# Performance work log

Hardware: AMD Instinct MI355X
Metric: run time of the kernel (lower is better)

The kernel has to match this reference:

```python
import jax, jax.numpy as jnp
import numpy as np

LOG2PI = float(np.log(2.0 * np.pi))


def setup_inputs() -> dict:
    key = jax.random.key(0)
    ks = jax.random.split(key, 5)
    B, T, XD, C = 128, 2050, 6, 64
    return {
        "x": jax.random.normal(ks[0], (B, T, XD), jnp.float32),
        "observation_means": jax.random.uniform(ks[1], (C, XD), dtype=jnp.float32),
        "observation_stddevs": jax.random.uniform(ks[2], (C, XD), dtype=jnp.float32),
        "log_A": jax.random.normal(ks[3], (C, C), jnp.float32),
        "log_pi": jax.random.normal(ks[4], (C,), jnp.float32),
    }


def _emission_logprob(x, means, stds):
    # Normal(means[:, :4], relu(stds[:, :4]) + 0.1).log_prob(x[:, :, :4]) summed over feat dim
    mu = means[:, :4]                       # (C,4)
    sigma = jax.nn.relu(stds[:, :4]) + 0.1  # (C,4)
    z = (x[:, :, None, :4] - mu) / sigma    # (B,T,C,4)
    return jnp.sum(-0.5 * z * z - jnp.log(sigma) - 0.5 * LOG2PI, axis=-1)  # (B,T,C)


def _forward_scalers(logp, log_A, log_pi):
    # scaled HMM forward pass; returns per-step log normalizers (T,B)
    a0 = logp[:, 0] + log_pi
    s0 = jax.nn.logsumexp(a0, axis=-1)
    a0n = a0 - s0[:, None]

    def step(a_prev, lp_t):
        a = lp_t + jax.nn.logsumexp(a_prev[:, :, None] + log_A[None], axis=1)
        s = jax.nn.logsumexp(a, axis=-1)
        return a - s[:, None], s

    _, s_rest = jax.lax.scan(step, a0n, jnp.swapaxes(logp[:, 1:], 0, 1))
    return jnp.concatenate([s0[None], s_rest], axis=0)  # (T,B)


def _viterbi(logp, log_A, log_pi):
    d0 = logp[:, 0] + log_pi  # (B,C)

    def step(d_prev, lp_t):
        scores = d_prev[:, :, None] + log_A[None]  # (B,C_prev,C_cur)
        psi_t = jnp.argmax(scores, axis=1)
        d = jnp.max(scores, axis=1) + lp_t
        return d, psi_t

    d_last, psi = jax.lax.scan(step, d0, jnp.swapaxes(logp[:, 1:], 0, 1))  # psi: (T-1,B,C)
    c_last = jnp.argmax(d_last, axis=-1)  # (B,)

    def back(c_next, psi_t):
        c_t = jnp.take_along_axis(psi_t, c_next[:, None], axis=1)[:, 0]
        return c_t, c_t

    _, cs = jax.lax.scan(back, c_last, psi, reverse=True)  # (T-1,B)
    c = jnp.concatenate([cs, c_last[None]], axis=0)  # (T,B)
    return jnp.swapaxes(c, 0, 1)  # (B,T)


def reference(x, observation_means, observation_stddevs, log_A, log_pi):
    logA = jax.nn.log_softmax(log_A, axis=1)
    logpi = jax.nn.log_softmax(log_pi, axis=0)
    logp = _emission_logprob(x, observation_means, observation_stddevs)  # (B,T,C)
    scalers = _forward_scalers(logp, logA, logpi)                         # (T,B)
    logp_x = jnp.sum(scalers, axis=0)                                     # (B,)
    c_est = _viterbi(logp, logA, logpi)                                   # (B,T) int
    return logp_x, c_est
```

## Files before the change

kernel.cpp:

```cpp
#include <hip/hip_runtime.h>

#define T_LEN 2050
#define B_SZ 128
#define NCHUNK 33
#define HL2PI 0.91893853320467274178f

__device__ __forceinline__ float waveMax(float v) {
#pragma unroll
    for (int off = 32; off >= 1; off >>= 1)
        v = fmaxf(v, __shfl_xor(v, off, 64));
    return v;
}
__device__ __forceinline__ float waveSum(float v) {
#pragma unroll
    for (int off = 32; off >= 1; off >>= 1)
        v += __shfl_xor(v, off, 64);
    return v;
}
__device__ __forceinline__ void waveArgmax(float& v, int& idx) {
#pragma unroll
    for (int off = 32; off >= 1; off >>= 1) {
        float ov = __shfl_xor(v, off, 64);
        int   oi = __shfl_xor(idx, off, 64);
        if (ov > v || (ov == v && oi < idx)) { v = ov; idx = oi; }
    }
}
__device__ __forceinline__ void cfence() { asm volatile("" ::: "memory"); }

__device__ __forceinline__ float dppSumAll(float v) {
#define SSTEP(ctrl) { int t_ = __builtin_amdgcn_update_dpp(0, __float_as_int(v), ctrl, 0xf, 0xf, true); \
                      v = v + __int_as_float(t_); }
    SSTEP(0x111) SSTEP(0x112) SSTEP(0x114) SSTEP(0x118) SSTEP(0x142) SSTEP(0x143)
#undef SSTEP
    return __int_as_float(__builtin_amdgcn_readlane(__float_as_int(v), 63));
}
__device__ __forceinline__ float dppMaxAll(float v) {
#define MSTEP(ctrl) { int t_ = __builtin_amdgcn_update_dpp(__float_as_int(v), __float_as_int(v), ctrl, 0xf, 0xf, false); \
                      v = fmaxf(v, __int_as_float(t_)); }
    MSTEP(0x111) MSTEP(0x112) MSTEP(0x114) MSTEP(0x118) MSTEP(0x142) MSTEP(0x143)
#undef MSTEP
    return __int_as_float(__builtin_amdgcn_readlane(__float_as_int(v), 63));
}

extern "C" __global__ __launch_bounds__(64, 1)
void hmm_prep(const float* __restrict__ logA_in,
              const float* __restrict__ logpi_in,
              float* __restrict__ lAg,
              float* __restrict__ lpig)
{
    __shared__ float la[64 * 65];
    __shared__ float rowlse[64];
    const int j = threadIdx.x;
#pragma unroll
    for (int k = 0; k < 64; ++k)
        la[k * 65 + j] = logA_in[k * 64 + j];
    cfence();
    {
        float m = -1e30f;
#pragma unroll
        for (int k = 0; k < 64; ++k) m = fmaxf(m, la[j * 65 + k]);
        float s = 0.f;
#pragma unroll
        for (int k = 0; k < 64; ++k) s += expf(la[j * 65 + k] - m);
        rowlse[j] = m + logf(s);
    }
    cfence();
    {
        float v = logpi_in[j];
        float m = waveMax(v);
        float s = waveSum(expf(v - m));
        lpig[j] = v - (m + logf(s));
    }
    float4* o = (float4*)lAg;
#pragma unroll
    for (int k = 0; k < 16; ++k) {
        float4 v;
        v.x = la[(4 * k + 0) * 65 + j] - rowlse[4 * k + 0];
        v.y = la[(4 * k + 1) * 65 + j] - rowlse[4 * k + 1];
        v.z = la[(4 * k + 2) * 65 + j] - rowlse[4 * k + 2];
        v.w = la[(4 * k + 3) * 65 + j] - rowlse[4 * k + 3];
        o[j * 16 + k] = v;
    }
}

extern "C" __global__ __launch_bounds__(64, 1)
void hmm_main(const float* __restrict__ x,
              const float* __restrict__ means,
              const float* __restrict__ stds,
              const float* __restrict__ lAg,
              const float* __restrict__ lpig,
              float* __restrict__ out,
              float* __restrict__ dstore,
              int* __restrict__ c_last)
{
    __shared__ __align__(16) float xs[12304];
    __shared__ __align__(16) float pbuf[64];

    const int j   = threadIdx.x;
    const int bid = blockIdx.x;
    const bool is_fwd = (bid < B_SZ);
    const int b = is_fwd ? bid : bid - B_SZ;

    {
        const float4* xg4 = (const float4*)(x + (size_t)b * T_LEN * 6);
        float4* xs4 = (float4*)xs;
        for (int i = j; i < 3075; i += 64) xs4[i] = xg4[i];
    }
    float lpi = lpig[j];

    float mu0 = means[j * 6 + 0], mu1 = means[j * 6 + 1];
    float mu2 = means[j * 6 + 2], mu3 = means[j * 6 + 3];
    float sg0 = fmaxf(stds[j * 6 + 0], 0.f) + 0.1f;
    float sg1 = fmaxf(stds[j * 6 + 1], 0.f) + 0.1f;
    float sg2 = fmaxf(stds[j * 6 + 2], 0.f) + 0.1f;
    float sg3 = fmaxf(stds[j * 6 + 3], 0.f) + 0.1f;
    float ls0 = logf(sg0), ls1 = logf(sg1), ls2 = logf(sg2), ls3 = logf(sg3);

    const float4* pv = (const float4*)pbuf;

    if (is_fwd) {
        float Ac[64];
        {
            const float4* g = (const float4*)lAg;
#pragma unroll
            for (int k = 0; k < 16; ++k) {
                float4 v = g[j * 16 + k];
                Ac[4 * k + 0] = __expf(v.x); Ac[4 * k + 1] = __expf(v.y);
                Ac[4 * k + 2] = __expf(v.z); Ac[4 * k + 3] = __expf(v.w);
            }
        }
        float i0 = 1.f / sg0, i1 = 1.f / sg1, i2 = 1.f / sg2, i3 = 1.f / sg3;
        float cst = -(ls0 + ls1 + ls2 + ls3) - 4.f * HL2PI;

        float z0 = (xs[0] - mu0) * i0, z1 = (xs[1] - mu1) * i1;
        float z2 = (xs[2] - mu2) * i2, z3 = (xs[3] - mu3) * i3;
        float a0 = (cst - 0.5f * (z0 * z0 + z1 * z1 + z2 * z2 + z3 * z3)) + lpi;
        float mm0 = dppMaxAll(a0);
        float u0 = __expf(a0 - mm0);
        pbuf[j] = u0;
        float4 rr[16];
#pragma unroll
        for (int k = 0; k < 16; ++k) rr[k] = pv[k];
        float s0 = dppSumAll(u0);
        double acc = (double)(mm0 + __logf(s0));
        float rcp = 1.0f / s0;
        float lp1;
        {
            float y0 = (xs[6] - mu0) * i0, y1 = (xs[7] - mu1) * i1;
            float y2 = (xs[8] - mu2) * i2, y3 = (xs[9] - mu3) * i3;
            lp1 = cst - 0.5f * (y0 * y0 + y1 * y1 + y2 * y2 + y3 * y3);
        }
        float mm_c = dppMaxAll(lp1);
        float e_c  = __expf(lp1 - mm_c) * rcp;

#pragma unroll 1
        for (int t = 1; t < T_LEN; ++t) {
            int o = ((t + 1 < T_LEN) ? (t + 1) : t) * 6;
            float y0 = xs[o], y1 = xs[o + 1], y2 = xs[o + 2], y3 = xs[o + 3];

            float q0 = 0.f, q1 = 0.f, q2 = 0.f, q3 = 0.f;
#pragma unroll
            for (int k = 0; k < 16; ++k) {
                float4 pp = rr[k];
                q0 = fmaf(pp.x, Ac[4 * k + 0], q0);
                q1 = fmaf(pp.y, Ac[4 * k + 1], q1);
                q2 = fmaf(pp.z, Ac[4 * k + 2], q2);
                q3 = fmaf(pp.w, Ac[4 * k + 3], q3);
            }
            float q = (q0 + q1) + (q2 + q3);
            float u = q * e_c;

            pbuf[j] = u;
#pragma unroll
            for (int k = 0; k < 16; ++k) rr[k] = pv[k];

            float s = dppSumAll(u);
            acc += (double)(mm_c + __logf(s));
            rcp = 1.0f / s;
            float w0 = (y0 - mu0) * i0, w1 = (y1 - mu1) * i1;
            float w2 = (y2 - mu2) * i2, w3 = (y3 - mu3) * i3;
            float lpn = cst - 0.5f * (w0 * w0 + w1 * w1 + w2 * w2 + w3 * w3);
            float mmn = dppMaxAll(lpn);
            e_c  = __expf(lpn - mmn) * rcp;
            mm_c = mmn;
        }
        if (j == 0) out[b] = (float)acc;
    } else {
        float lA[64];
        {
            const float4* g = (const float4*)lAg;
#pragma unroll
            for (int k = 0; k < 16; ++k) {
                float4 v = g[j * 16 + k];
                lA[4 * k + 0] = v.x; lA[4 * k + 1] = v.y;
                lA[4 * k + 2] = v.z; lA[4 * k + 3] = v.w;
            }
        }
        float z0 = (xs[0] - mu0) / sg0, z1 = (xs[1] - mu1) / sg1;
        float z2 = (xs[2] - mu2) / sg2, z3 = (xs[3] - mu3) / sg3;
        float e0 = ((-0.5f * z0) * z0 - ls0) - HL2PI;
        float e1 = ((-0.5f * z1) * z1 - ls1) - HL2PI;
        float e2 = ((-0.5f * z2) * z2 - ls2) - HL2PI;
        float e3 = ((-0.5f * z3) * z3 - ls3) - HL2PI;
        float dn = (((e0 + e1) + e2) + e3) + lpi;
        pbuf[j] = dn;
        float4 rr[16];
#pragma unroll
        for (int k = 0; k < 16; ++k) rr[k] = pv[k];
        float* dp = dstore + (size_t)b * 64 + j;
        *dp = dn;
        float lp_c;
        {
            float y0 = (xs[6] - mu0) / sg0, y1 = (xs[7] - mu1) / sg1;
            float y2 = (xs[8] - mu2) / sg2, y3 = (xs[9] - mu3) / sg3;
            float f0 = ((-0.5f * y0) * y0 - ls0) - HL2PI;
            float f1 = ((-0.5f * y1) * y1 - ls1) - HL2PI;
            float f2 = ((-0.5f * y2) * y2 - ls2) - HL2PI;
            float f3 = ((-0.5f * y3) * y3 - ls3) - HL2PI;
            lp_c = ((f0 + f1) + f2) + f3;
        }

#pragma unroll 1
        for (int t = 1; t < T_LEN; ++t) {
            int o = ((t + 1 < T_LEN) ? (t + 1) : t) * 6;
            float y0 = xs[o], y1 = xs[o + 1], y2 = xs[o + 2], y3 = xs[o + 3];

            float m0 = -3.4e38f, m1 = -3.4e38f, m2 = -3.4e38f, m3 = -3.4e38f;
#pragma unroll
            for (int k = 0; k < 16; ++k) {
                float4 dd = rr[k];
                m0 = fmaxf(m0, dd.x + lA[4 * k + 0]);
                m1 = fmaxf(m1, dd.y + lA[4 * k + 1]);
                m2 = fmaxf(m2, dd.z + lA[4 * k + 2]);
                m3 = fmaxf(m3, dd.w + lA[4 * k + 3]);
            }
            float best = fmaxf(fmaxf(m0, m1), fmaxf(m2, m3));
            dn = best + lp_c;

            pbuf[j] = dn;
#pragma unroll
            for (int k = 0; k < 16; ++k) rr[k] = pv[k];

            dp += B_SZ * 64;
            *dp = dn;
            float w0 = (y0 - mu0) / sg0, w1 = (y1 - mu1) / sg1;
            float w2 = (y2 - mu2) / sg2, w3 = (y3 - mu3) / sg3;
            float f0 = ((-0.5f * w0) * w0 - ls0) - HL2PI;
            float f1 = ((-0.5f * w1) * w1 - ls1) - HL2PI;
            float f2 = ((-0.5f * w2) * w2 - ls2) - HL2PI;
            float f3 = ((-0.5f * w3) * w3 - ls3) - HL2PI;
            lp_c = ((f0 + f1) + f2) + f3;
        }

        float vv = dn; int idx = j;
        waveArgmax(vv, idx);
        if (j == 0) c_last[b] = idx;
    }
}

extern "C" __global__ __launch_bounds__(256)
void hmm_psi(const float* __restrict__ dstore,
             const float* __restrict__ lAg,
             unsigned char* __restrict__ psi)
{
    __shared__ __align__(16) float sd[4][64];
    const int warp = threadIdx.x >> 6;
    const int j = threadIdx.x & 63;
    const int wid = blockIdx.x * 4 + warp;

    float lA[64];
    {
        const float4* g = (const float4*)lAg;
#pragma unroll
        for (int k = 0; k < 16; ++k) {
            float4 v = g[j * 16 + k];
            lA[4 * k + 0] = v.x; lA[4 * k + 1] = v.y;
            lA[4 * k + 2] = v.z; lA[4 * k + 3] = v.w;
        }
    }
    const float4* dv = (const float4*)sd[warp];
    const int NP = 2049 * B_SZ;

    for (int p = wid; p < NP; p += 2048) {
        const int t = (p >> 7) + 1;
        const int b = p & 127;
        float dval = dstore[((size_t)(t - 1) * B_SZ + b) * 64 + j];
        sd[warp][j] = dval;

        float bv0 = -3.4e38f, bv1 = -3.4e38f, bv2 = -3.4e38f, bv3 = -3.4e38f;
        int bi0 = 0, bi1 = 1, bi2 = 2, bi3 = 3;
#pragma unroll
        for (int k = 0; k < 16; ++k) {
            float4 dd = dv[k];
            float v0 = dd.x + lA[4 * k + 0];
            float v1 = dd.y + lA[4 * k + 1];
            float v2 = dd.z + lA[4 * k + 2];
            float v3 = dd.w + lA[4 * k + 3];
            if (v0 > bv0) { bv0 = v0; bi0 = 4 * k + 0; }
            if (v1 > bv1) { bv1 = v1; bi1 = 4 * k + 1; }
            if (v2 > bv2) { bv2 = v2; bi2 = 4 * k + 2; }
            if (v3 > bv3) { bv3 = v3; bi3 = 4 * k + 3; }
        }
        float best = bv0; int bidx = bi0;
        if (bv1 > best || (bv1 == best && bi1 < bidx)) { best = bv1; bidx = bi1; }
        if (bv2 > best || (bv2 == best && bi2 < bidx)) { best = bv2; bidx = bi2; }
        if (bv3 > best || (bv3 == best && bi3 < bidx)) { best = bv3; bidx = bi3; }

        psi[((size_t)t * B_SZ + b) * 64 + j] = (unsigned char)bidx;
    }
}

extern "C" __global__ __launch_bounds__(256)
void hmm_compose(const unsigned char* __restrict__ psi,
                 unsigned char* __restrict__ mt)
{
    const int w = blockIdx.x * 4 + (threadIdx.x >> 6);
    const int j = threadIdx.x & 63;
    const int g = w % NCHUNK;
    const int b = w / NCHUNK;
    const int e = (g < NCHUNK - 1) ? g * 64 + 64 : (T_LEN - 1);
    int M = j;
    for (int t = e; t >= g * 64 + 1; --t)
        M = psi[((size_t)t * B_SZ + b) * 64 + M];
    mt[((size_t)g * B_SZ + b) * 64 + j] = (unsigned char)M;
}

extern "C" __global__ __launch_bounds__(64, 1)
void hmm_fill(const unsigned char* __restrict__ psi,
              const unsigned char* __restrict__ mt,
              const int* __restrict__ c_last,
              float* __restrict__ out)
{
    __shared__ int sb[NCHUNK];
    const int b = blockIdx.x;
    const int g = threadIdx.x;
    const int cl = c_last[b];
    if (g == 0) {
        int cur = cl;
        for (int q = NCHUNK - 1; q >= 0; --q) {
            cur = mt[((size_t)q * B_SZ + b) * 64 + cur];
            sb[q] = cur;
        }
    }
    cfence();
    float* oc = out + B_SZ + (size_t)b * T_LEN;
    if (g == NCHUNK) {
        oc[T_LEN - 1] = (float)cl;
    } else if (g < NCHUNK) {
        const int e = (g < NCHUNK - 1) ? g * 64 + 64 : (T_LEN - 1);
        int s = (g < NCHUNK - 1) ? sb[g + 1] : cl;
        for (int t = e; t >= g * 64 + 1; --t) {
            s = psi[((size_t)t * B_SZ + b) * 64 + s];
            oc[t - 1] = (float)s;
        }
    }
}

extern "C" void kernel_launch(void* const* d_in, const int* in_sizes, int n_in,
                              void* d_out, int out_size, void* d_ws, size_t ws_size,
                              hipStream_t stream)
{
    const float* x      = (const float*)d_in[0];
    const float* means  = (const float*)d_in[1];
    const float* stds   = (const float*)d_in[2];
    const float* logA   = (const float*)d_in[3];
    const float* logpi  = (const float*)d_in[4];
    float* out = (float*)d_out;

    char* base = (char*)d_ws;
    float*         dstore = (float*)base;
    unsigned char* psi    = (unsigned char*)(base + 67174400);
    unsigned char* mt     = (unsigned char*)(base + 83968000);
    int*           cl     = (int*)(base + 84238336);
    float*         lAg    = (float*)(base + 84238848);
    float*         lpig   = (float*)(base + 84255232);

    hipLaunchKernelGGL(hmm_prep, dim3(1), dim3(64), 0, stream, logA, logpi, lAg, lpig);
    hipLaunchKernelGGL(hmm_main, dim3(2 * B_SZ), dim3(64), 0, stream,
                       x, means, stds, lAg, lpig, out, dstore, cl);
    hipLaunchKernelGGL(hmm_psi, dim3(512), dim3(256), 0, stream, dstore, lAg, psi);
    hipLaunchKernelGGL(hmm_compose, dim3((NCHUNK * B_SZ) / 4), dim3(256), 0, stream, psi, mt);
    hipLaunchKernelGGL(hmm_fill, dim3(B_SZ), dim3(64), 0, stream, psi, mt, cl, out);
}
```

Measured before the change: 1.078 ms.

## Fuse forward and Viterbi recurrences into one wave per batch; widen psi grid

```diff
diff --git a/kernel.cpp b/kernel.cpp
--- a/kernel.cpp
+++ b/kernel.cpp
@@ -94,12 +94,11 @@
               int* __restrict__ c_last)
 {
     __shared__ __align__(16) float xs[12304];
-    __shared__ __align__(16) float pbuf[64];
-
-    const int j   = threadIdx.x;
-    const int bid = blockIdx.x;
-    const bool is_fwd = (bid < B_SZ);
-    const int b = is_fwd ? bid : bid - B_SZ;
+    __shared__ __align__(16) float fbuf[64];
+    __shared__ __align__(16) float vbuf[64];
+
+    const int j = threadIdx.x;
+    const int b = blockIdx.x;
 
     {
         const float4* xg4 = (const float4*)(x + (size_t)b * T_LEN * 6);
@@ -116,146 +115,126 @@
     float sg3 = fmaxf(stds[j * 6 + 3], 0.f) + 0.1f;
     float ls0 = logf(sg0), ls1 = logf(sg1), ls2 = logf(sg2), ls3 = logf(sg3);
 
-    const float4* pv = (const float4*)pbuf;
-
-    if (is_fwd) {
-        float Ac[64];
-        {
-            const float4* g = (const float4*)lAg;
-#pragma unroll
-            for (int k = 0; k < 16; ++k) {
-                float4 v = g[j * 16 + k];
-                Ac[4 * k + 0] = __expf(v.x); Ac[4 * k + 1] = __expf(v.y);
-                Ac[4 * k + 2] = __expf(v.z); Ac[4 * k + 3] = __expf(v.w);
-            }
-        }
-        float i0 = 1.f / sg0, i1 = 1.f / sg1, i2 = 1.f / sg2, i3 = 1.f / sg3;
-        float cst = -(ls0 + ls1 + ls2 + ls3) - 4.f * HL2PI;
-
-        float z0 = (xs[0] - mu0) * i0, z1 = (xs[1] - mu1) * i1;
-        float z2 = (xs[2] - mu2) * i2, z3 = (xs[3] - mu3) * i3;
-        float a0 = (cst - 0.5f * (z0 * z0 + z1 * z1 + z2 * z2 + z3 * z3)) + lpi;
-        float mm0 = dppMaxAll(a0);
-        float u0 = __expf(a0 - mm0);
-        pbuf[j] = u0;
-        float4 rr[16];
-#pragma unroll
-        for (int k = 0; k < 16; ++k) rr[k] = pv[k];
-        float s0 = dppSumAll(u0);
-        double acc = (double)(mm0 + __logf(s0));
-        float rcp = 1.0f / s0;
-        float lp1;
-        {
-            float y0 = (xs[6] - mu0) * i0, y1 = (xs[7] - mu1) * i1;
-            float y2 = (xs[8] - mu2) * i2, y3 = (xs[9] - mu3) * i3;
-            lp1 = cst - 0.5f * (y0 * y0 + y1 * y1 + y2 * y2 + y3 * y3);
-        }
-        float mm_c = dppMaxAll(lp1);
-        float e_c  = __expf(lp1 - mm_c) * rcp;
+    float lA[64], Ac[64];
+    {
+        const float4* g = (const float4*)lAg;
+#pragma unroll
+        for (int k = 0; k < 16; ++k) {
+            float4 v = g[j * 16 + k];
+            lA[4 * k + 0] = v.x; lA[4 * k + 1] = v.y;
+            lA[4 * k + 2] = v.z; lA[4 * k + 3] = v.w;
+        }
+#pragma unroll
+        for (int k = 0; k < 64; ++k) Ac[k] = __expf(lA[k]);
+    }
+    float i0 = 1.f / sg0, i1 = 1.f / sg1, i2 = 1.f / sg2, i3 = 1.f / sg3;
+    float cst = -(ls0 + ls1 + ls2 + ls3) - 4.f * HL2PI;
+
+    const float4* fv = (const float4*)fbuf;
+    const float4* vv = (const float4*)vbuf;
+
+    float z0 = (xs[0] - mu0) * i0, z1 = (xs[1] - mu1) * i1;
+    float z2 = (xs[2] - mu2) * i2, z3 = (xs[3] - mu3) * i3;
+    float a0 = (cst - 0.5f * (z0 * z0 + z1 * z1 + z2 * z2 + z3 * z3)) + lpi;
+    float mm0 = dppMaxAll(a0);
+    float u = __expf(a0 - mm0);
+    fbuf[j] = u;
+    float v0 = (xs[0] - mu0) / sg0, v1 = (xs[1] - mu1) / sg1;
+    float v2 = (xs[2] - mu2) / sg2, v3 = (xs[3] - mu3) / sg3;
+    float e0 = ((-0.5f * v0) * v0 - ls0) - HL2PI;
+    float e1 = ((-0.5f * v1) * v1 - ls1) - HL2PI;
+    float e2 = ((-0.5f * v2) * v2 - ls2) - HL2PI;
+    float e3 = ((-0.5f * v3) * v3 - ls3) - HL2PI;
+    float dn = (((e0 + e1) + e2) + e3) + lpi;
+    vbuf[j] = dn;
+
+    float4 fr[16], vr[16];
+#pragma unroll
+    for (int k = 0; k < 16; ++k) fr[k] = fv[k];
+#pragma unroll
+    for (int k = 0; k < 16; ++k) vr[k] = vv[k];
+
+    float s0 = dppSumAll(u);
+    double acc = (double)(mm0 + __logf(s0));
+    float rcp = 1.0f / s0;
+    float* dp = dstore + (size_t)b * 64 + j;
+    *dp = dn;
+
+    float lp_f, mm_c, e_c, lp_v;
+    {
+        float y0 = xs[6], y1 = xs[7], y2 = xs[8], y3 = xs[9];
+        float w0 = (y0 - mu0) * i0, w1 = (y1 - mu1) * i1;
+        float w2 = (y2 - mu2) * i2, w3 = (y3 - mu3) * i3;
+        lp_f = cst - 0.5f * (w0 * w0 + w1 * w1 + w2 * w2 + w3 * w3);
+        mm_c = dppMaxAll(lp_f);
+        e_c  = __expf(lp_f - mm_c) * rcp;
+        float q0 = (y0 - mu0) / sg0, q1 = (y1 - mu1) / sg1;
+        float q2 = (y2 - mu2) / sg2, q3 = (y3 - mu3) / sg3;
+        float f0 = ((-0.5f * q0) * q0 - ls0) - HL2PI;
+        float f1 = ((-0.5f * q1) * q1 - ls1) - HL2PI;
+        float f2 = ((-0.5f * q2) * q2 - ls2) - HL2PI;
+        float f3 = ((-0.5f * q3) * q3 - ls3) - HL2PI;
+        lp_v = ((f0 + f1) + f2) + f3;
+    }
 
 #pragma unroll 1
-        for (int t = 1; t < T_LEN; ++t) {
-            int o = ((t + 1 < T_LEN) ? (t + 1) : t) * 6;
-            float y0 = xs[o], y1 = xs[o + 1], y2 = xs[o + 2], y3 = xs[o + 3];
-
-            float q0 = 0.f, q1 = 0.f, q2 = 0.f, q3 = 0.f;
-#pragma unroll
-            for (int k = 0; k < 16; ++k) {
-                float4 pp = rr[k];
-                q0 = fmaf(pp.x, Ac[4 * k + 0], q0);
-                q1 = fmaf(pp.y, Ac[4 * k + 1], q1);
-                q2 = fmaf(pp.z, Ac[4 * k + 2], q2);
-                q3 = fmaf(pp.w, Ac[4 * k + 3], q3);
-            }
-            float q = (q0 + q1) + (q2 + q3);
-            float u = q * e_c;
-
-            pbuf[j] = u;
-#pragma unroll
-            for (int k = 0; k < 16; ++k) rr[k] = pv[k];
-
-            float s = dppSumAll(u);
-            acc += (double)(mm_c + __logf(s));
-            rcp = 1.0f / s;
-            float w0 = (y0 - mu0) * i0, w1 = (y1 - mu1) * i1;
-            float w2 = (y2 - mu2) * i2, w3 = (y3 - mu3) * i3;
-            float lpn = cst - 0.5f * (w0 * w0 + w1 * w1 + w2 * w2 + w3 * w3);
-            float mmn = dppMaxAll(lpn);
-            e_c  = __expf(lpn - mmn) * rcp;
-            mm_c = mmn;
-        }
-        if (j == 0) out[b] = (float)acc;
-    } else {
-        float lA[64];
-        {
-            const float4* g = (const float4*)lAg;
-#pragma unroll
-            for (int k = 0; k < 16; ++k) {
-                float4 v = g[j * 16 + k];
-                lA[4 * k + 0] = v.x; lA[4 * k + 1] = v.y;
-                lA[4 * k + 2] = v.z; lA[4 * k + 3] = v.w;
-            }
-        }
-        float z0 = (xs[0] - mu0) / sg0, z1 = (xs[1] - mu1) / sg1;
-        float z2 = (xs[2] - mu2) / sg2, z3 = (xs[3] - mu3) / sg3;
-        float e0 = ((-0.5f * z0) * z0 - ls0) - HL2PI;
-        float e1 = ((-0.5f * z1) * z1 - ls1) - HL2PI;
-        float e2 = ((-0.5f * z2) * z2 - ls2) - HL2PI;
-        float e3 = ((-0.5f * z3) * z3 - ls3) - HL2PI;
-        float dn = (((e0 + e1) + e2) + e3) + lpi;
-        pbuf[j] = dn;
-        float4 rr[16];
-#pragma unroll
-        for (int k = 0; k < 16; ++k) rr[k] = pv[k];
-        float* dp = dstore + (size_t)b * 64 + j;
+    for (int t = 1; t < T_LEN; ++t) {
+        int o = ((t + 1 < T_LEN) ? (t + 1) : t) * 6;
+        float y0 = xs[o], y1 = xs[o + 1], y2 = xs[o + 2], y3 = xs[o + 3];
+
+        float m0 = -3.4e38f, m1 = -3.4e38f, m2 = -3.4e38f, m3 = -3.4e38f;
+#pragma unroll
+        for (int k = 0; k < 16; ++k) {
+            float4 dd = vr[k];
+            m0 = fmaxf(m0, dd.x + lA[4 * k + 0]);
+            m1 = fmaxf(m1, dd.y + lA[4 * k + 1]);
+            m2 = fmaxf(m2, dd.z + lA[4 * k + 2]);
+            m3 = fmaxf(m3, dd.w + lA[4 * k + 3]);
+        }
+        dn = fmaxf(fmaxf(m0, m1), fmaxf(m2, m3)) + lp_v;
+
+        float q0 = 0.f, q1 = 0.f, q2 = 0.f, q3 = 0.f;
+#pragma unroll
+        for (int k = 0; k < 16; ++k) {
+            float4 pp = fr[k];
+            q0 = fmaf(pp.x, Ac[4 * k + 0], q0);
+            q1 = fmaf(pp.y, Ac[4 * k + 1], q1);
+            q2 = fmaf(pp.z, Ac[4 * k + 2], q2);
+            q3 = fmaf(pp.w, Ac[4 * k + 3], q3);
+        }
+        u = ((q0 + q1) + (q2 + q3)) * e_c;
+
+        vbuf[j] = dn;
+        fbuf[j] = u;
+#pragma unroll
+        for (int k = 0; k < 16; ++k) vr[k] = vv[k];
+#pragma unroll
+        for (int k = 0; k < 16; ++k) fr[k] = fv[k];
+
+        dp += B_SZ * 64;
         *dp = dn;
-        float lp_c;
-        {
-            float y0 = (xs[6] - mu0) / sg0, y1 = (xs[7] - mu1) / sg1;
-            float y2 = (xs[8] - mu2) / sg2, y3 = (xs[9] - mu3) / sg3;
-            float f0 = ((-0.5f * y0) * y0 - ls0) - HL2PI;
-            float f1 = ((-0.5f * y1) * y1 - ls1) - HL2PI;
-            float f2 = ((-0.5f * y2) * y2 - ls2) - HL2PI;
-            float f3 = ((-0.5f * y3) * y3 - ls3) - HL2PI;
-            lp_c = ((f0 + f1) + f2) + f3;
-        }
-
-#pragma unroll 1
-        for (int t = 1; t < T_LEN; ++t) {
-            int o = ((t + 1 < T_LEN) ? (t + 1) : t) * 6;
-            float y0 = xs[o], y1 = xs[o + 1], y2 = xs[o + 2], y3 = xs[o + 3];
-
-            float m0 = -3.4e38f, m1 = -3.4e38f, m2 = -3.4e38f, m3 = -3.4e38f;
-#pragma unroll
-            for (int k = 0; k < 16; ++k) {
-                float4 dd = rr[k];
-                m0 = fmaxf(m0, dd.x + lA[4 * k + 0]);
-                m1 = fmaxf(m1, dd.y + lA[4 * k + 1]);
-                m2 = fmaxf(m2, dd.z + lA[4 * k + 2]);
-                m3 = fmaxf(m3, dd.w + lA[4 * k + 3]);
-            }
-            float best = fmaxf(fmaxf(m0, m1), fmaxf(m2, m3));
-            dn = best + lp_c;
-
-            pbuf[j] = dn;
-#pragma unroll
-            for (int k = 0; k < 16; ++k) rr[k] = pv[k];
-
-            dp += B_SZ * 64;
-            *dp = dn;
-            float w0 = (y0 - mu0) / sg0, w1 = (y1 - mu1) / sg1;
-            float w2 = (y2 - mu2) / sg2, w3 = (y3 - mu3) / sg3;
-            float f0 = ((-0.5f * w0) * w0 - ls0) - HL2PI;
-            float f1 = ((-0.5f * w1) * w1 - ls1) - HL2PI;
-            float f2 = ((-0.5f * w2) * w2 - ls2) - HL2PI;
-            float f3 = ((-0.5f * w3) * w3 - ls3) - HL2PI;
-            lp_c = ((f0 + f1) + f2) + f3;
-        }
-
-        float vv = dn; int idx = j;
-        waveArgmax(vv, idx);
-        if (j == 0) c_last[b] = idx;
-    }
+        float s = dppSumAll(u);
+        acc += (double)(mm_c + __logf(s));
+        rcp = 1.0f / s;
+        float w0 = (y0 - mu0) * i0, w1 = (y1 - mu1) * i1;
+        float w2 = (y2 - mu2) * i2, w3 = (y3 - mu3) * i3;
+        float lpn = cst - 0.5f * (w0 * w0 + w1 * w1 + w2 * w2 + w3 * w3);
+        float mmn = dppMaxAll(lpn);
+        e_c  = __expf(lpn - mmn) * rcp;
+        mm_c = mmn;
+        float x0 = (y0 - mu0) / sg0, x1 = (y1 - mu1) / sg1;
+        float x2 = (y2 - mu2) / sg2, x3 = (y3 - mu3) / sg3;
+        float f0 = ((-0.5f * x0) * x0 - ls0) - HL2PI;
+        float f1 = ((-0.5f * x1) * x1 - ls1) - HL2PI;
+        float f2 = ((-0.5f * x2) * x2 - ls2) - HL2PI;
+        float f3 = ((-0.5f * x3) * x3 - ls3) - HL2PI;
+        lp_v = ((f0 + f1) + f2) + f3;
+    }
+
+    if (j == 0) out[b] = (float)acc;
+    float vvx = dn; int idx = j;
+    waveArgmax(vvx, idx);
+    if (j == 0) c_last[b] = idx;
 }
 
 extern "C" __global__ __launch_bounds__(256)
@@ -281,7 +260,7 @@
     const float4* dv = (const float4*)sd[warp];
     const int NP = 2049 * B_SZ;
 
-    for (int p = wid; p < NP; p += 2048) {
+    for (int p = wid; p < NP; p += 8192) {
         const int t = (p >> 7) + 1;
         const int b = p & 127;
         float dval = dstore[((size_t)(t - 1) * B_SZ + b) * 64 + j];
@@ -376,9 +355,9 @@
     float*         lpig   = (float*)(base + 84255232);
 
     hipLaunchKernelGGL(hmm_prep, dim3(1), dim3(64), 0, stream, logA, logpi, lAg, lpig);
-    hipLaunchKernelGGL(hmm_main, dim3(2 * B_SZ), dim3(64), 0, stream,
+    hipLaunchKernelGGL(hmm_main, dim3(B_SZ), dim3(64), 0, stream,
                        x, means, stds, lAg, lpig, out, dstore, cl);
-    hipLaunchKernelGGL(hmm_psi, dim3(512), dim3(256), 0, stream, dstore, lAg, psi);
+    hipLaunchKernelGGL(hmm_psi, dim3(2048), dim3(256), 0, stream, dstore, lAg, psi);
     hipLaunchKernelGGL(hmm_compose, dim3((NCHUNK * B_SZ) / 4), dim3(256), 0, stream, psi, mt);
     hipLaunchKernelGGL(hmm_fill, dim3(B_SZ), dim3(64), 0, stream, psi, mt, cl, out);
 }
```

After: 1.859 ms. 72.4% more time.

## Replace LDS broadcast with readlane, precompute emissions, defer forward normalization

Applied to the files above, without the earlier changes.

```diff
diff --git a/kernel.cpp b/kernel.cpp
--- a/kernel.cpp
+++ b/kernel.cpp
@@ -40,6 +40,9 @@
     MSTEP(0x111) MSTEP(0x112) MSTEP(0x114) MSTEP(0x118) MSTEP(0x142) MSTEP(0x143)
 #undef MSTEP
     return __int_as_float(__builtin_amdgcn_readlane(__float_as_int(v), 63));
+}
+__device__ __forceinline__ float rlane(int bits, int lane) {
+    return __int_as_float(__builtin_amdgcn_readlane(bits, lane));
 }
 
 extern "C" __global__ __launch_bounds__(64, 1)
@@ -83,6 +86,39 @@
     }
 }
 
+extern "C" __global__ __launch_bounds__(256)
+void hmm_emis(const float* __restrict__ x,
+              const float* __restrict__ means,
+              const float* __restrict__ stds,
+              float* __restrict__ buf)
+{
+    const int wid = blockIdx.x * 4 + (threadIdx.x >> 6);
+    const int j = threadIdx.x & 63;
+    const int t = wid >> 7;
+    const int b = wid & 127;
+
+    const float* xt = x + ((size_t)b * T_LEN + t) * 6;
+    float x0 = xt[0], x1 = xt[1], x2 = xt[2], x3 = xt[3];
+
+    float mu0 = means[j * 6 + 0], mu1 = means[j * 6 + 1];
+    float mu2 = means[j * 6 + 2], mu3 = means[j * 6 + 3];
+    float sg0 = fmaxf(stds[j * 6 + 0], 0.f) + 0.1f;
+    float sg1 = fmaxf(stds[j * 6 + 1], 0.f) + 0.1f;
+    float sg2 = fmaxf(stds[j * 6 + 2], 0.f) + 0.1f;
+    float sg3 = fmaxf(stds[j * 6 + 3], 0.f) + 0.1f;
+    float ls0 = logf(sg0), ls1 = logf(sg1), ls2 = logf(sg2), ls3 = logf(sg3);
+
+    float z0 = (x0 - mu0) / sg0, z1 = (x1 - mu1) / sg1;
+    float z2 = (x2 - mu2) / sg2, z3 = (x3 - mu3) / sg3;
+    float e0 = ((-0.5f * z0) * z0 - ls0) - HL2PI;
+    float e1 = ((-0.5f * z1) * z1 - ls1) - HL2PI;
+    float e2 = ((-0.5f * z2) * z2 - ls2) - HL2PI;
+    float e3 = ((-0.5f * z3) * z3 - ls3) - HL2PI;
+    float lp = ((e0 + e1) + e2) + e3;
+
+    buf[((size_t)b * T_LEN + t) * 64 + j] = lp;
+}
+
 extern "C" __global__ __launch_bounds__(64, 1)
 void hmm_main(const float* __restrict__ x,
               const float* __restrict__ means,
@@ -90,35 +126,34 @@
               const float* __restrict__ lAg,
               const float* __restrict__ lpig,
               float* __restrict__ out,
-              float* __restrict__ dstore,
+              float* __restrict__ buf,
               int* __restrict__ c_last)
 {
     __shared__ __align__(16) float xs[12304];
-    __shared__ __align__(16) float pbuf[64];
 
     const int j   = threadIdx.x;
     const int bid = blockIdx.x;
     const bool is_fwd = (bid < B_SZ);
     const int b = is_fwd ? bid : bid - B_SZ;
 
-    {
-        const float4* xg4 = (const float4*)(x + (size_t)b * T_LEN * 6);
-        float4* xs4 = (float4*)xs;
-        for (int i = j; i < 3075; i += 64) xs4[i] = xg4[i];
-    }
     float lpi = lpig[j];
 
-    float mu0 = means[j * 6 + 0], mu1 = means[j * 6 + 1];
-    float mu2 = means[j * 6 + 2], mu3 = means[j * 6 + 3];
-    float sg0 = fmaxf(stds[j * 6 + 0], 0.f) + 0.1f;
-    float sg1 = fmaxf(stds[j * 6 + 1], 0.f) + 0.1f;
-    float sg2 = fmaxf(stds[j * 6 + 2], 0.f) + 0.1f;
-    float sg3 = fmaxf(stds[j * 6 + 3], 0.f) + 0.1f;
-    float ls0 = logf(sg0), ls1 = logf(sg1), ls2 = logf(sg2), ls3 = logf(sg3);
-
-    const float4* pv = (const float4*)pbuf;
-
     if (is_fwd) {
+        {
+            const float4* xg4 = (const float4*)(x + (size_t)b * T_LEN * 6);
+            float4* xs4 = (float4*)xs;
+            for (int i = j; i < 3075; i += 64) xs4[i] = xg4[i];
+        }
+        float mu0 = means[j * 6 + 0], mu1 = means[j * 6 + 1];
+        float mu2 = means[j * 6 + 2], mu3 = means[j * 6 + 3];
+        float sg0 = fmaxf(stds[j * 6 + 0], 0.f) + 0.1f;
+        float sg1 = fmaxf(stds[j * 6 + 1], 0.f) + 0.1f;
+        float sg2 = fmaxf(stds[j * 6 + 2], 0.f) + 0.1f;
+        float sg3 = fmaxf(stds[j * 6 + 3], 0.f) + 0.1f;
+        float ls0 = logf(sg0), ls1 = logf(sg1), ls2 = logf(sg2), ls3 = logf(sg3);
+        float i0 = 1.f / sg0, i1 = 1.f / sg1, i2 = 1.f / sg2, i3 = 1.f / sg3;
+        float cst = -(ls0 + ls1 + ls2 + ls3) - 4.f * HL2PI;
+
         float Ac[64];
         {
             const float4* g = (const float4*)lAg;
@@ -129,61 +164,58 @@
                 Ac[4 * k + 2] = __expf(v.z); Ac[4 * k + 3] = __expf(v.w);
             }
         }
-        float i0 = 1.f / sg0, i1 = 1.f / sg1, i2 = 1.f / sg2, i3 = 1.f / sg3;
-        float cst = -(ls0 + ls1 + ls2 + ls3) - 4.f * HL2PI;
+        cfence();
 
         float z0 = (xs[0] - mu0) * i0, z1 = (xs[1] - mu1) * i1;
         float z2 = (xs[2] - mu2) * i2, z3 = (xs[3] - mu3) * i3;
         float a0 = (cst - 0.5f * (z0 * z0 + z1 * z1 + z2 * z2 + z3 * z3)) + lpi;
-        float mm0 = dppMaxAll(a0);
-        float u0 = __expf(a0 - mm0);
-        pbuf[j] = u0;
-        float4 rr[16];
-#pragma unroll
-        for (int k = 0; k < 16; ++k) rr[k] = pv[k];
-        float s0 = dppSumAll(u0);
-        double acc = (double)(mm0 + __logf(s0));
-        float rcp = 1.0f / s0;
-        float lp1;
+        float m0a = dppMaxAll(a0);
+        float u = __expf(a0 - m0a);
+        float s0 = dppSumAll(u);
+        double acc = (double)(m0a + __logf(s0));
+        u *= (1.0f / s0);
+
+        float mm_c, e_c;
         {
             float y0 = (xs[6] - mu0) * i0, y1 = (xs[7] - mu1) * i1;
             float y2 = (xs[8] - mu2) * i2, y3 = (xs[9] - mu3) * i3;
-            lp1 = cst - 0.5f * (y0 * y0 + y1 * y1 + y2 * y2 + y3 * y3);
-        }
-        float mm_c = dppMaxAll(lp1);
-        float e_c  = __expf(lp1 - mm_c) * rcp;
+            float lp1 = cst - 0.5f * (y0 * y0 + y1 * y1 + y2 * y2 + y3 * y3);
+            mm_c = dppMaxAll(lp1);
+            e_c  = __expf(lp1 - mm_c);
+        }
 
 #pragma unroll 1
         for (int t = 1; t < T_LEN; ++t) {
             int o = ((t + 1 < T_LEN) ? (t + 1) : t) * 6;
             float y0 = xs[o], y1 = xs[o + 1], y2 = xs[o + 2], y3 = xs[o + 3];
 
+            int ub = __float_as_int(u);
             float q0 = 0.f, q1 = 0.f, q2 = 0.f, q3 = 0.f;
 #pragma unroll
             for (int k = 0; k < 16; ++k) {
-                float4 pp = rr[k];
-                q0 = fmaf(pp.x, Ac[4 * k + 0], q0);
-                q1 = fmaf(pp.y, Ac[4 * k + 1], q1);
-                q2 = fmaf(pp.z, Ac[4 * k + 2], q2);
-                q3 = fmaf(pp.w, Ac[4 * k + 3], q3);
+                q0 = fmaf(rlane(ub, 4 * k + 0), Ac[4 * k + 0], q0);
+                q1 = fmaf(rlane(ub, 4 * k + 1), Ac[4 * k + 1], q1);
+                q2 = fmaf(rlane(ub, 4 * k + 2), Ac[4 * k + 2], q2);
+                q3 = fmaf(rlane(ub, 4 * k + 3), Ac[4 * k + 3], q3);
             }
             float q = (q0 + q1) + (q2 + q3);
-            float u = q * e_c;
-
-            pbuf[j] = u;
-#pragma unroll
-            for (int k = 0; k < 16; ++k) rr[k] = pv[k];
-
-            float s = dppSumAll(u);
-            acc += (double)(mm_c + __logf(s));
-            rcp = 1.0f / s;
+            u = q * e_c;
+            acc += (double)mm_c;
+            if ((t & 3) == 0) {
+                float ss = dppSumAll(u);
+                acc += (double)__logf(ss);
+                u *= (1.0f / ss);
+            }
+
             float w0 = (y0 - mu0) * i0, w1 = (y1 - mu1) * i1;
             float w2 = (y2 - mu2) * i2, w3 = (y3 - mu3) * i3;
             float lpn = cst - 0.5f * (w0 * w0 + w1 * w1 + w2 * w2 + w3 * w3);
             float mmn = dppMaxAll(lpn);
-            e_c  = __expf(lpn - mmn) * rcp;
+            e_c  = __expf(lpn - mmn);
             mm_c = mmn;
         }
+        float sf = dppSumAll(u);
+        acc += (double)__logf(sf);
         if (j == 0) out[b] = (float)acc;
     } else {
         float lA[64];
@@ -196,60 +228,38 @@
                 lA[4 * k + 2] = v.z; lA[4 * k + 3] = v.w;
             }
         }
-        float z0 = (xs[0] - mu0) / sg0, z1 = (xs[1] - mu1) / sg1;
-        float z2 = (xs[2] - mu2) / sg2, z3 = (xs[3] - mu3) / sg3;
-        float e0 = ((-0.5f * z0) * z0 - ls0) - HL2PI;
-        float e1 = ((-0.5f * z1) * z1 - ls1) - HL2PI;
-        float e2 = ((-0.5f * z2) * z2 - ls2) - HL2PI;
-        float e3 = ((-0.5f * z3) * z3 - ls3) - HL2PI;
-        float dn = (((e0 + e1) + e2) + e3) + lpi;
-        pbuf[j] = dn;
-        float4 rr[16];
-#pragma unroll
-        for (int k = 0; k < 16; ++k) rr[k] = pv[k];
-        float* dp = dstore + (size_t)b * 64 + j;
-        *dp = dn;
-        float lp_c;
-        {
-            float y0 = (xs[6] - mu0) / sg0, y1 = (xs[7] - mu1) / sg1;
-            float y2 = (xs[8] - mu2) / sg2, y3 = (xs[9] - mu3) / sg3;
-            float f0 = ((-0.5f * y0) * y0 - ls0) - HL2PI;
-            float f1 = ((-0.5f * y1) * y1 - ls1) - HL2PI;
-            float f2 = ((-0.5f * y2) * y2 - ls2) - HL2PI;
-            float f3 = ((-0.5f * y3) * y3 - ls3) - HL2PI;
-            lp_c = ((f0 + f1) + f2) + f3;
-        }
+        float* bb = buf + (size_t)b * T_LEN * 64 + j;
+
+        float dn = bb[0] + lpi;
+        float l0 = bb[64], l1 = bb[128], l2 = bb[192], l3 = bb[256];
+        bb[0] = dn;
 
 #pragma unroll 1
         for (int t = 1; t < T_LEN; ++t) {
-            int o = ((t + 1 < T_LEN) ? (t + 1) : t) * 6;
-            float y0 = xs[o], y1 = xs[o + 1], y2 = xs[o + 2], y3 = xs[o + 3];
-
+            float lp_c = l0; l0 = l1; l1 = l2; l2 = l3;
+            int tp = t + 4; if (tp > T_LEN - 1) tp = T_LEN - 1;
+            l3 = bb[(size_t)tp * 64];
+
+            int db = __float_as_int(dn);
             float m0 = -3.4e38f, m1 = -3.4e38f, m2 = -3.4e38f, m3 = -3.4e38f;
 #pragma unroll
-            for (int k = 0; k < 16; ++k) {
-                float4 dd = rr[k];
-                m0 = fmaxf(m0, dd.x + lA[4 * k + 0]);
-                m1 = fmaxf(m1, dd.y + lA[4 * k + 1]);
-                m2 = fmaxf(m2, dd.z + lA[4 * k + 2]);
-                m3 = fmaxf(m3, dd.w + lA[4 * k + 3]);
+            for (int k = 0; k < 8; ++k) {
+                float t0 = rlane(db, 8 * k + 0) + lA[8 * k + 0];
+                float t1 = rlane(db, 8 * k + 1) + lA[8 * k + 1];
+                float t2 = rlane(db, 8 * k + 2) + lA[8 * k + 2];
+                float t3 = rlane(db, 8 * k + 3) + lA[8 * k + 3];
+                float t4 = rlane(db, 8 * k + 4) + lA[8 * k + 4];
+                float t5 = rlane(db, 8 * k + 5) + lA[8 * k + 5];
+                float t6 = rlane(db, 8 * k + 6) + lA[8 * k + 6];
+                float t7 = rlane(db, 8 * k + 7) + lA[8 * k + 7];
+                m0 = fmaxf(fmaxf(m0, t0), t1);
+                m1 = fmaxf(fmaxf(m1, t2), t3);
+                m2 = fmaxf(fmaxf(m2, t4), t5);
+                m3 = fmaxf(fmaxf(m3, t6), t7);
             }
             float best = fmaxf(fmaxf(m0, m1), fmaxf(m2, m3));
             dn = best + lp_c;
-
-            pbuf[j] = dn;
-#pragma unroll
-            for (int k = 0; k < 16; ++k) rr[k] = pv[k];
-
-            dp += B_SZ * 64;
-            *dp = dn;
-            float w0 = (y0 - mu0) / sg0, w1 = (y1 - mu1) / sg1;
-            float w2 = (y2 - mu2) / sg2, w3 = (y3 - mu3) / sg3;
-            float f0 = ((-0.5f * w0) * w0 - ls0) - HL2PI;
-            float f1 = ((-0.5f * w1) * w1 - ls1) - HL2PI;
-            float f2 = ((-0.5f * w2) * w2 - ls2) - HL2PI;
-            float f3 = ((-0.5f * w3) * w3 - ls3) - HL2PI;
-            lp_c = ((f0 + f1) + f2) + f3;
+            bb[(size_t)t * 64] = dn;
         }
 
         float vv = dn; int idx = j;
@@ -259,7 +269,7 @@
 }
 
 extern "C" __global__ __launch_bounds__(256)
-void hmm_psi(const float* __restrict__ dstore,
+void hmm_psi(const float* __restrict__ buf,
              const float* __restrict__ lAg,
              unsigned char* __restrict__ psi)
 {
@@ -281,10 +291,10 @@
     const float4* dv = (const float4*)sd[warp];
     const int NP = 2049 * B_SZ;
 
-    for (int p = wid; p < NP; p += 2048) {
+    for (int p = wid; p < NP; p += 8192) {
         const int t = (p >> 7) + 1;
         const int b = p & 127;
-        float dval = dstore[((size_t)(t - 1) * B_SZ + b) * 64 + j];
+        float dval = buf[((size_t)b * T_LEN + (t - 1)) * 64 + j];
         sd[warp][j] = dval;
 
         float bv0 = -3.4e38f, bv1 = -3.4e38f, bv2 = -3.4e38f, bv3 = -3.4e38f;
@@ -368,17 +378,19 @@
     float* out = (float*)d_out;
 
     char* base = (char*)d_ws;
-    float*         dstore = (float*)base;
-    unsigned char* psi    = (unsigned char*)(base + 67174400);
-    unsigned char* mt     = (unsigned char*)(base + 83968000);
-    int*           cl     = (int*)(base + 84238336);
-    float*         lAg    = (float*)(base + 84238848);
-    float*         lpig   = (float*)(base + 84255232);
+    float*         buf  = (float*)base;
+    unsigned char* psi  = (unsigned char*)(base + 67174400);
+    unsigned char* mt   = (unsigned char*)(base + 83968000);
+    int*           cl   = (int*)(base + 84238336);
+    float*         lAg  = (float*)(base + 84238848);
+    float*         lpig = (float*)(base + 84255232);
 
     hipLaunchKernelGGL(hmm_prep, dim3(1), dim3(64), 0, stream, logA, logpi, lAg, lpig);
+    hipLaunchKernelGGL(hmm_emis, dim3((T_LEN * B_SZ) / 4), dim3(256), 0, stream,
+                       x, means, stds, buf);
     hipLaunchKernelGGL(hmm_main, dim3(2 * B_SZ), dim3(64), 0, stream,
-                       x, means, stds, lAg, lpig, out, dstore, cl);
-    hipLaunchKernelGGL(hmm_psi, dim3(512), dim3(256), 0, stream, dstore, lAg, psi);
+                       x, means, stds, lAg, lpig, out, buf, cl);
+    hipLaunchKernelGGL(hmm_psi, dim3(2048), dim3(256), 0, stream, buf, lAg, psi);
     hipLaunchKernelGGL(hmm_compose, dim3((NCHUNK * B_SZ) / 4), dim3(256), 0, stream, psi, mt);
     hipLaunchKernelGGL(hmm_fill, dim3(B_SZ), dim3(64), 0, stream, psi, mt, cl, out);
 }
```

New measurement: 1.059 ms. No clear change (-1.7%).
